# Optimization experiments

Hardware: AMD Instinct MI355X
Metric: run time of the kernel (lower is better)

## Reference

```python
import jax, jax.numpy as jnp
import numpy as np

H = 128
IN = 5
EPS = 1e-5


def lstm(x, Wih, Whh, bih, bhh):
    # x: [B,T,D]; PyTorch gate order i,f,g,o along 4H axis
    B, T, _ = x.shape
    xW = jnp.einsum('btd,gd->btg', x, Wih) + bih + bhh  # [B,T,4H]
    WhhT = Whh.T

    def step(carry, xt):
        h, c = carry
        g = xt + h @ WhhT
        i, f, gg, o = jnp.split(g, 4, axis=-1)
        i = jax.nn.sigmoid(i)
        f = jax.nn.sigmoid(f)
        gg = jnp.tanh(gg)
        o = jax.nn.sigmoid(o)
        c = f * c + i * gg
        h = o * jnp.tanh(c)
        return (h, c), h

    h0 = jnp.zeros((B, H), x.dtype)
    _, hs = jax.lax.scan(step, (h0, h0), jnp.swapaxes(xW, 0, 1))
    return jnp.swapaxes(hs, 0, 1)  # [B,T,H]


def batchnorm(x, gamma, beta):
    # training-mode BN over (batch, time) per channel; x: [B,T,H]
    mean = jnp.mean(x, axis=(0, 1))
    var = jnp.var(x, axis=(0, 1))
    return (x - mean) * (gamma * jax.lax.rsqrt(var + EPS)) + beta


def forward_one(x, Wih1, Whh1, bih1, bhh1, g1, b1, Wih2, Whh2, bih2, bhh2, g2, b2, fcW, fcb):
    out = lstm(x, Wih1, Whh1, bih1, bhh1)
    out = batchnorm(out, g1, b1)
    # dropout is identity (eval / deterministic reference)
    out = lstm(out, Wih2, Whh2, bih2, bhh2)
    out = batchnorm(out, g2, b2)
    emb = out[:, -1, :] @ fcW.T + fcb  # [B,128]
    norm = jnp.sqrt(jnp.sum(emb * emb, axis=1, keepdims=True))
    return emb / jnp.maximum(norm, 1e-12)  # F.normalize p=2


def setup_inputs() -> dict:
    key = jax.random.key(0)
    ks = jax.random.split(key, 20)
    B, T = 512, 128
    s_in = 1.0 / np.sqrt(H)
    d = {
        'a': jax.random.normal(ks[0], (B, T, IN), jnp.float32),
        'p': jax.random.normal(ks[1], (B, T, IN), jnp.float32),
        'n': jax.random.normal(ks[2], (B, T, IN), jnp.float32),
        'Wih1': jax.random.uniform(ks[3], (4 * H, IN), jnp.float32, -s_in, s_in),
        'Whh1': jax.random.uniform(ks[4], (4 * H, H), jnp.float32, -s_in, s_in),
        'bih1': jax.random.uniform(ks[5], (4 * H,), jnp.float32, -s_in, s_in),
        'bhh1': jax.random.uniform(ks[6], (4 * H,), jnp.float32, -s_in, s_in),
        'g1': jnp.ones((H,), jnp.float32),
        'b1': jnp.zeros((H,), jnp.float32),
        'Wih2': jax.random.uniform(ks[7], (4 * H, H), jnp.float32, -s_in, s_in),
        'Whh2': jax.random.uniform(ks[8], (4 * H, H), jnp.float32, -s_in, s_in),
        'bih2': jax.random.uniform(ks[9], (4 * H,), jnp.float32, -s_in, s_in),
        'bhh2': jax.random.uniform(ks[10], (4 * H,), jnp.float32, -s_in, s_in),
        'g2': jnp.ones((H,), jnp.float32),
        'b2': jnp.zeros((H,), jnp.float32),
        'fcW': jax.random.uniform(ks[11], (H, H), jnp.float32, -s_in, s_in),
        'fcb': jax.random.uniform(ks[12], (H,), jnp.float32, -s_in, s_in),
    }
    return d


def reference(a, p, n, Wih1, Whh1, bih1, bhh1, g1, b1, Wih2, Whh2, bih2, bhh2, g2, b2, fcW, fcb):
    f = lambda x: forward_one(x, Wih1, Whh1, bih1, bhh1, g1, b1, Wih2, Whh2, bih2, bhh2, g2, b2, fcW, fcb)
    return (f(a), f(p), f(n))
```

## Files before the change

kernel.cpp:

```cpp
#include <hip/hip_runtime.h>


typedef __attribute__((ext_vector_type(8))) _Float16 half8;
typedef __attribute__((ext_vector_type(4))) float f32x4;

#define TS 128
#define HID 128
#define NGATE 512
#define INV_N (1.0f/65536.0f)

#define BAR() asm volatile("s_waitcnt lgkmcnt(0)\n\ts_barrier" ::: "memory")

__device__ __forceinline__ float rcpf(float x) { return __builtin_amdgcn_rcpf(x); }
__device__ __forceinline__ float clamp20(float x) { return fminf(fmaxf(x, -20.0f), 20.0f); }

__device__ __forceinline__ _Float16 lstm_cell(float zi, float zf, float zg, float zo,
                                              float& c) {
  zg = clamp20(zg);
  float ei = __expf(-zi);
  float eg = __expf(-2.0f * zg);
  float ef = __expf(-zf);
  float fv = rcpf(1.0f + ef);
  float ig = (1.0f - eg) * rcpf((1.0f + ei) * (1.0f + eg));
  float cc = fv * c + ig;
  c = cc;
  float ccl = clamp20(cc);
  float eo = __expf(-zo);
  float ec = __expf(-2.0f * ccl);
  float hv = (1.0f - ec) * rcpf((1.0f + eo) * (1.0f + ec));
  return (_Float16)hv;
}


__global__ __launch_bounds__(512, 2) void lstm1_kernel(
    const float* __restrict__ xa, const float* __restrict__ xp,
    const float* __restrict__ xn,
    const float* __restrict__ Wih1, const float* __restrict__ Whh1,
    const float* __restrict__ bih1, const float* __restrict__ bhh1,
    _Float16* __restrict__ hs1,
    float* __restrict__ s1part, float* __restrict__ s1qpart) {
  const int wg = blockIdx.x;
  const int inp = wg >> 5;
  const int tid = threadIdx.x;
  const int w = tid >> 6;
  const int lane = tid & 63;
  const int l15 = lane & 15;
  const int quad = lane >> 4;
  const int col = w * 16 + l15;
  const int kb = quad * 8;

  __shared__ _Float16 hb[2][2048];
  __shared__ _Float16 xt[TS][128];

  const float* x = (inp == 0) ? xa : ((inp == 1) ? xp : xn);
  const int rloc = (wg & 31) * 16;

  for (int i = tid; i < 4096; i += 512) ((_Float16*)hb)[i] = (_Float16)0.0f;
  for (int i = tid; i < TS * 128; i += 512) ((_Float16*)xt)[i] = (_Float16)0.0f;
  __syncthreads();
  for (int i = tid; i < 10240; i += 512) {
    int r = i / 640, rem = i - r * 640;
    int t = rem / 5, d = rem - t * 5;
    xt[t][r * 8 + d] = (_Float16)x[(rloc + r) * 640 + rem];
  }

  half8 bh[4][4];
#pragma unroll
  for (int kt = 0; kt < 4; ++kt)
#pragma unroll
    for (int gt = 0; gt < 4; ++gt) {
      const float* src = &Whh1[(gt * 128 + col) * HID + kt * 32 + kb];
      half8 v;
#pragma unroll
      for (int j = 0; j < 8; ++j) v[j] = (_Float16)src[j];
      bh[kt][gt] = v;
    }
  half8 bx[4];
#pragma unroll
  for (int gt = 0; gt < 4; ++gt) {
    half8 v = {0, 0, 0, 0, 0, 0, 0, 0};
    if (quad == 0) {
#pragma unroll
      for (int j = 0; j < 5; ++j) v[j] = (_Float16)Wih1[(gt * 128 + col) * 5 + j];
    }
    bx[gt] = v;
  }
  f32x4 biasv[4];
#pragma unroll
  for (int gt = 0; gt < 4; ++gt) {
    float b = bih1[gt * 128 + col] + bhh1[gt * 128 + col];
    biasv[gt][0] = b; biasv[gt][1] = b; biasv[gt][2] = b; biasv[gt][3] = b;
  }

  const int rbase = (quad * 16 + l15) * 8;
  const int wbase = (w >> 1) * 512 + ((w & 1) * 2 + (l15 >> 3)) * 128 +
                    quad * 32 + (l15 & 7);
  _Float16* hs1w = hs1 + (size_t)wg * TS * 2048;

  float c[4] = {0, 0, 0, 0};
  float ssum = 0.0f, ssq = 0.0f;
  __syncthreads();

  half8 xv = {0, 0, 0, 0, 0, 0, 0, 0};
  if (quad == 0) xv = *(const half8*)&xt[0][l15 * 8];

  for (int t = 0; t < TS; ++t) {
    f32x4 acc[4];
#pragma unroll
    for (int gt = 0; gt < 4; ++gt)
      acc[gt] = __builtin_amdgcn_mfma_f32_16x16x32_f16(xv, bx[gt], biasv[gt], 0, 0, 0);
    if (t + 1 < TS && quad == 0)
      xv = *(const half8*)&xt[t + 1][l15 * 8];
    BAR();
    if (t > 0) {
      float2 cp = *(const float2*)&hb[t & 1][tid * 4];
      *(float2*)&hs1w[(size_t)(t - 1) * 2048 + tid * 4] = cp;
    }
#pragma unroll
    for (int kt = 0; kt < 4; ++kt) {
      half8 ah = *(const half8*)&hb[t & 1][kt * 512 + rbase];
#pragma unroll
      for (int gt = 0; gt < 4; ++gt)
        acc[gt] = __builtin_amdgcn_mfma_f32_16x16x32_f16(ah, bh[kt][gt], acc[gt], 0, 0, 0);
    }
    const int wb = (t + 1) & 1;
#pragma unroll
    for (int r = 0; r < 4; ++r) {
      _Float16 hh = lstm_cell(acc[0][r], acc[1][r], acc[2][r], acc[3][r], c[r]);
      float hr = (float)hh;
      ssum += hr; ssq += hr * hr;
      hb[wb][wbase + r * 8] = hh;
    }
  }
  BAR();
  {
    float2 cp = *(const float2*)&hb[0][tid * 4];
    *(float2*)&hs1w[(size_t)(TS - 1) * 2048 + tid * 4] = cp;
  }
  float s = ssum, q = ssq;
  s += __shfl_xor(s, 16); s += __shfl_xor(s, 32);
  q += __shfl_xor(q, 16); q += __shfl_xor(q, 32);
  if (quad == 0) {
    s1part[wg * HID + col] = s;
    s1qpart[wg * HID + col] = q;
  }
}

__global__ void mid_kernel(const float* __restrict__ s1part, const float* __restrict__ s1qpart,
                           const float* __restrict__ g1, const float* __restrict__ b1,
                           const float* __restrict__ Wih2,
                           const float* __restrict__ bih2, const float* __restrict__ bhh2,
                           _Float16* __restrict__ w2s, float* __restrict__ bias2eff) {
  int bid = blockIdx.x, tid = threadIdx.x;
  if (bid < 768) {
    int i0 = bid * 256;
    int inp = i0 >> 16, k = (i0 & 65535) >> 9;
    __shared__ float red[65];
    if (tid < 32) {
      red[tid] = s1part[(inp * 32 + tid) * HID + k];
      red[32 + tid] = s1qpart[(inp * 32 + tid) * HID + k];
    }
    __syncthreads();
    if (tid == 0) {
      float sm = 0.0f, sq = 0.0f;
      for (int j = 0; j < 32; ++j) { sm += red[j]; sq += red[32 + j]; }
      float m = sm * INV_N;
      float v = sq * INV_N - m * m;
      red[64] = g1[k] * rsqrtf(v + 1e-5f);
    }
    __syncthreads();
    float sc = red[64];
    int i = i0 + tid, g = i & 511;
    w2s[i] = (_Float16)(sc * Wih2[g * HID + k]);
  } else {
    int i = (bid - 768) * 256 + tid;
    int inp = i >> 9, g = i & 511;
    __shared__ float sc[128], sh[128];
    if (tid < 128) {
      float sm = 0.0f, sq = 0.0f;
      for (int j = 0; j < 32; ++j) {
        sm += s1part[(inp * 32 + j) * HID + tid];
        sq += s1qpart[(inp * 32 + j) * HID + tid];
      }
      float m = sm * INV_N;
      float v = sq * INV_N - m * m;
      float s = g1[tid] * rsqrtf(v + 1e-5f);
      sc[tid] = s;
      sh[tid] = b1[tid] - m * s;
    }
    __syncthreads();
    float acc = bih2[g] + bhh2[g];
    for (int h = 0; h < HID; ++h) acc += sh[h] * Wih2[g * HID + h];
    bias2eff[i] = acc;
  }
}

__global__ __launch_bounds__(512, 2) void lstm2_kernel(
    const _Float16* __restrict__ hs1,
    const _Float16* __restrict__ w2s,
    const float* __restrict__ Whh2,
    const float* __restrict__ bias2eff,
    _Float16* __restrict__ hlast,
    float* __restrict__ s2part, float* __restrict__ s2qpart) {
  const int wg = blockIdx.x;
  const int inp = wg >> 5;
  const int tid = threadIdx.x;
  const int w = tid >> 6;
  const int lane = tid & 63;
  const int l15 = lane & 15;
  const int quad = lane >> 4;
  const int col = w * 16 + l15;
  const int kb = quad * 8;

  __shared__ _Float16 hb[2][2048];
  for (int i = tid; i < 4096; i += 512) ((_Float16*)hb)[i] = (_Float16)0.0f;

  const _Float16* w2sI = w2s + (size_t)inp * HID * NGATE;
  half8 bh[4][4], bxw[4][4];
#pragma unroll
  for (int kt = 0; kt < 4; ++kt)
#pragma unroll
    for (int gt = 0; gt < 4; ++gt) {
      int gcol = gt * 128 + col;
      const float* ph = &Whh2[(size_t)gcol * HID + kt * 32 + kb];
      half8 vh, vx;
#pragma unroll
      for (int j = 0; j < 8; ++j) {
        vh[j] = (_Float16)ph[j];
        vx[j] = w2sI[(kt * 32 + kb + j) * NGATE + gcol];
      }
      bh[kt][gt] = vh;
      bxw[kt][gt] = vx;
    }
  f32x4 biasv[4];
#pragma unroll
  for (int gt = 0; gt < 4; ++gt) {
    float b = bias2eff[inp * NGATE + gt * 128 + col];
    biasv[gt][0] = b; biasv[gt][1] = b; biasv[gt][2] = b; biasv[gt][3] = b;
  }

  const int rbase = (quad * 16 + l15) * 8;
  const int wbase = (w >> 1) * 512 + ((w & 1) * 2 + (l15 >> 3)) * 128 +
                    quad * 32 + (l15 & 7);
  const _Float16* hg = hs1 + (size_t)wg * TS * 2048;

  half8 a2A[4], a2B[4];
#pragma unroll
  for (int kt = 0; kt < 4; ++kt) {
    a2A[kt] = *(const half8*)&hg[kt * 512 + rbase];
    a2B[kt] = *(const half8*)&hg[(size_t)2048 + kt * 512 + rbase];
  }

  float c[4] = {0, 0, 0, 0};
  float ssum = 0.0f, ssq = 0.0f;

  __syncthreads();

  auto step = [&](int t, half8 (&cur)[4]) {
    f32x4 acc[4];
#pragma unroll
    for (int gt = 0; gt < 4; ++gt)
      acc[gt] = __builtin_amdgcn_mfma_f32_16x16x32_f16(cur[0], bxw[0][gt], biasv[gt], 0, 0, 0);
#pragma unroll
    for (int kt = 1; kt < 4; ++kt)
#pragma unroll
      for (int gt = 0; gt < 4; ++gt)
        acc[gt] = __builtin_amdgcn_mfma_f32_16x16x32_f16(cur[kt], bxw[kt][gt], acc[gt], 0, 0, 0);
    if (t + 2 < TS) {
#pragma unroll
      for (int kt = 0; kt < 4; ++kt)
        cur[kt] = *(const half8*)&hg[(size_t)(t + 2) * 2048 + kt * 512 + rbase];
    }
    BAR();
#pragma unroll
    for (int kt = 0; kt < 4; ++kt) {
      half8 ah = *(const half8*)&hb[t & 1][kt * 512 + rbase];
#pragma unroll
      for (int gt = 0; gt < 4; ++gt)
        acc[gt] = __builtin_amdgcn_mfma_f32_16x16x32_f16(ah, bh[kt][gt], acc[gt], 0, 0, 0);
    }
    const int wb = (t + 1) & 1;
#pragma unroll
    for (int r = 0; r < 4; ++r) {
      _Float16 hh = lstm_cell(acc[0][r], acc[1][r], acc[2][r], acc[3][r], c[r]);
      float hr = (float)hh;
      ssum += hr; ssq += hr * hr;
      hb[wb][wbase + r * 8] = hh;
    }
  };

  for (int t = 0; t < TS; t += 2) {
    step(t, a2A);
    step(t + 1, a2B);
  }

  BAR();
  {
    float2 cp = *(const float2*)&hb[0][tid * 4];
    *(float2*)&hlast[(size_t)wg * 2048 + tid * 4] = cp;
  }
  float s = ssum, q = ssq;
  s += __shfl_xor(s, 16); s += __shfl_xor(s, 32);
  q += __shfl_xor(q, 16); q += __shfl_xor(q, 32);
  if (quad == 0) {
    s2part[wg * HID + col] = s;
    s2qpart[wg * HID + col] = q;
  }
}

__global__ __launch_bounds__(256, 1) void head_kernel(
    const _Float16* __restrict__ hlast,
    const float* __restrict__ s2part, const float* __restrict__ s2qpart,
    const float* __restrict__ g2, const float* __restrict__ b2,
    const float* __restrict__ fcW, const float* __restrict__ fcb,
    float* __restrict__ out) {
  const int wg = blockIdx.x;
  const int inp = wg >> 5;
  const int gr0 = wg * 16;
  const int tid = threadIdx.x;

  __shared__ float fcwT[128][132];
  __shared__ float bnh[16][132];
  __shared__ float s2[128], sh2[128];
  __shared__ float part[16][16];
  __shared__ float inv[16];

  if (tid < 128) {
    float sm = 0.0f, sq = 0.0f;
    for (int j = 0; j < 32; ++j) {
      sm += s2part[(inp * 32 + j) * HID + tid];
      sq += s2qpart[(inp * 32 + j) * HID + tid];
    }
    float m = sm * INV_N;
    float v = sq * INV_N - m * m;
    float s = g2[tid] * rsqrtf(v + 1e-5f);
    s2[tid] = s; sh2[tid] = b2[tid] - m * s;
  }
  for (int i = tid; i < 16384; i += 256) {
    int j = i >> 7, h = i & 127;
    fcwT[h][j] = fcW[i];
  }
  __syncthreads();
  {
    int row = tid >> 4, c0 = (tid & 15) * 8;
#pragma unroll
    for (int k = 0; k < 8; ++k) {
      int h = c0 + k;
      int ad = ((h >> 5) << 9) + (((h >> 3) & 3) << 7) + (row << 3) + (h & 7);
      bnh[row][h] = (float)hlast[(size_t)wg * 2048 + ad] * s2[h] + sh2[h];
    }
  }
  __syncthreads();
  const int row = tid >> 4, jl = tid & 15;
  float emb[8];
  float sq = 0.0f;
#pragma unroll
  for (int jj = 0; jj < 8; ++jj) {
    int j = jl + jj * 16;
    float acc = fcb[j];
    for (int h = 0; h < HID; ++h) acc += bnh[row][h] * fcwT[h][j];
    emb[jj] = acc; sq += acc * acc;
  }
  part[row][jl] = sq;
  __syncthreads();
  if (tid < 16) {
    float s = 0.0f;
    for (int k = 0; k < 16; ++k) s += part[tid][k];
    inv[tid] = 1.0f / fmaxf(sqrtf(s), 1e-12f);
  }
  __syncthreads();
#pragma unroll
  for (int jj = 0; jj < 8; ++jj)
    out[(size_t)(gr0 + row) * HID + jl + jj * 16] = emb[jj] * inv[row];
}

extern "C" void kernel_launch(void* const* d_in, const int* in_sizes, int n_in,
                              void* d_out, int out_size, void* d_ws, size_t ws_size,
                              hipStream_t stream) {
  const float* a    = (const float*)d_in[0];
  const float* p    = (const float*)d_in[1];
  const float* nn   = (const float*)d_in[2];
  const float* Wih1 = (const float*)d_in[3];
  const float* Whh1 = (const float*)d_in[4];
  const float* bih1 = (const float*)d_in[5];
  const float* bhh1 = (const float*)d_in[6];
  const float* g1   = (const float*)d_in[7];
  const float* b1   = (const float*)d_in[8];
  const float* Wih2 = (const float*)d_in[9];
  const float* Whh2 = (const float*)d_in[10];
  const float* bih2 = (const float*)d_in[11];
  const float* bhh2 = (const float*)d_in[12];
  const float* g2   = (const float*)d_in[13];
  const float* b2   = (const float*)d_in[14];
  const float* fcW  = (const float*)d_in[15];
  const float* fcb  = (const float*)d_in[16];

  char* ws = (char*)d_ws;
  float* s1part  = (float*)(ws + 0);
  float* s1qpart = (float*)(ws + 49152);
  float* s2part  = (float*)(ws + 98304);
  float* s2qpart = (float*)(ws + 147456);
  _Float16* w2s   = (_Float16*)(ws + 196608);
  float* bias2eff = (float*)(ws + 589824);
  _Float16* hlast = (_Float16*)(ws + 595968);
  _Float16* hs1   = (_Float16*)(ws + 989184);


  lstm1_kernel<<<96, 512, 0, stream>>>(a, p, nn, Wih1, Whh1, bih1, bhh1,
                                       hs1, s1part, s1qpart);
  mid_kernel<<<774, 256, 0, stream>>>(s1part, s1qpart, g1, b1, Wih2, bih2, bhh2,
                                      w2s, bias2eff);
  lstm2_kernel<<<96, 512, 0, stream>>>(hs1, w2s, Whh2, bias2eff,
                                       hlast, s2part, s2qpart);
  head_kernel<<<96, 256, 0, stream>>>(hlast, s2part, s2qpart, g2, b2, fcW, fcb,
                                      (float*)d_out);
}
```

Measured before the change: 375.1 us.

## Add prep kernel for padded x and transposed fp16 weights; split MFMA accumulation chains

A new prep kernel converts the inputs to a padded fp16 layout, transposes Whh1/Whh2 to fp16, and presums the layer-1 biases. lstm1 then streams x directly from global memory instead of staging it in LDS with a serial zero-fill and scatter. Both LSTM kernels split the recurrent MFMA chain into two independent accumulators that are summed at the end, shortening the dependent MFMA latency on each time step's critical path. The cost is an extra kernel launch with large global writes, plus per-step global loads of x in lstm1 in place of LDS reads.

```diff
diff --git a/kernel.cpp b/kernel.cpp
--- a/kernel.cpp
+++ b/kernel.cpp
@@ -32,15 +32,41 @@
 }
 
 
+__global__ void prep_all(const float* __restrict__ xa, const float* __restrict__ xp,
+                         const float* __restrict__ xn,
+                         const float* __restrict__ Whh1, const float* __restrict__ Whh2,
+                         const float* __restrict__ bih1, const float* __restrict__ bhh1,
+                         _Float16* __restrict__ xpad,
+                         _Float16* __restrict__ whhT1, _Float16* __restrict__ whhT2,
+                         float* __restrict__ b1c) {
+  int bid = blockIdx.x, tid = threadIdx.x;
+  if (bid < 6144) {
+    int i = bid * 256 + tid;
+    int tile = i >> 14, rem = i & 16383;
+    int t = rem >> 7, r = (rem >> 3) & 15, d = i & 7;
+    int inp = tile >> 5, rloc = (tile & 31) * 16;
+    const float* x = (inp == 0) ? xa : ((inp == 1) ? xp : xn);
+    xpad[i] = (d < 5) ? (_Float16)x[(rloc + r) * 640 + t * 5 + d] : (_Float16)0.0f;
+  } else if (bid < 6656) {
+    int i = (bid - 6144) * 256 + tid;
+    int which = i >> 16, idx = i & 65535;
+    int k = idx >> 9, g = idx & 511;
+    const float* src = which ? Whh2 : Whh1;
+    (which ? whhT2 : whhT1)[idx] = (_Float16)src[g * HID + k];
+  } else {
+    int i = (bid - 6656) * 256 + tid;
+    b1c[i] = bih1[i] + bhh1[i];
+  }
+}
+
 __global__ __launch_bounds__(512, 2) void lstm1_kernel(
-    const float* __restrict__ xa, const float* __restrict__ xp,
-    const float* __restrict__ xn,
-    const float* __restrict__ Wih1, const float* __restrict__ Whh1,
-    const float* __restrict__ bih1, const float* __restrict__ bhh1,
+    const _Float16* __restrict__ xpad,
+    const float* __restrict__ Wih1,
+    const float* __restrict__ b1c,
+    const _Float16* __restrict__ whhT,
     _Float16* __restrict__ hs1,
     float* __restrict__ s1part, float* __restrict__ s1qpart) {
   const int wg = blockIdx.x;
-  const int inp = wg >> 5;
   const int tid = threadIdx.x;
   const int w = tid >> 6;
   const int lane = tid & 63;
@@ -50,29 +76,17 @@
   const int kb = quad * 8;
 
   __shared__ _Float16 hb[2][2048];
-  __shared__ _Float16 xt[TS][128];
-
-  const float* x = (inp == 0) ? xa : ((inp == 1) ? xp : xn);
-  const int rloc = (wg & 31) * 16;
-
   for (int i = tid; i < 4096; i += 512) ((_Float16*)hb)[i] = (_Float16)0.0f;
-  for (int i = tid; i < TS * 128; i += 512) ((_Float16*)xt)[i] = (_Float16)0.0f;
-  __syncthreads();
-  for (int i = tid; i < 10240; i += 512) {
-    int r = i / 640, rem = i - r * 640;
-    int t = rem / 5, d = rem - t * 5;
-    xt[t][r * 8 + d] = (_Float16)x[(rloc + r) * 640 + rem];
-  }
 
   half8 bh[4][4];
 #pragma unroll
   for (int kt = 0; kt < 4; ++kt)
 #pragma unroll
     for (int gt = 0; gt < 4; ++gt) {
-      const float* src = &Whh1[(gt * 128 + col) * HID + kt * 32 + kb];
+      int gcol = gt * 128 + col;
       half8 v;
 #pragma unroll
-      for (int j = 0; j < 8; ++j) v[j] = (_Float16)src[j];
+      for (int j = 0; j < 8; ++j) v[j] = whhT[(kt * 32 + kb + j) * NGATE + gcol];
       bh[kt][gt] = v;
     }
   half8 bx[4];
@@ -88,9 +102,10 @@
   f32x4 biasv[4];
 #pragma unroll
   for (int gt = 0; gt < 4; ++gt) {
-    float b = bih1[gt * 128 + col] + bhh1[gt * 128 + col];
+    float b = b1c[gt * 128 + col];
     biasv[gt][0] = b; biasv[gt][1] = b; biasv[gt][2] = b; biasv[gt][3] = b;
   }
+  const f32x4 zero4 = {0, 0, 0, 0};
 
   const int rbase = (quad * 16 + l15) * 8;
   const int wbase = (w >> 1) * 512 + ((w & 1) * 2 + (l15 >> 3)) * 128 +
@@ -102,7 +117,7 @@
   __syncthreads();
 
   half8 xv = {0, 0, 0, 0, 0, 0, 0, 0};
-  if (quad == 0) xv = *(const half8*)&xt[0][l15 * 8];
+  if (quad == 0) xv = *(const half8*)&xpad[((size_t)(wg * TS) * 16 + l15) * 8];
 
   for (int t = 0; t < TS; ++t) {
     f32x4 acc[4];
@@ -110,19 +125,32 @@
     for (int gt = 0; gt < 4; ++gt)
       acc[gt] = __builtin_amdgcn_mfma_f32_16x16x32_f16(xv, bx[gt], biasv[gt], 0, 0, 0);
     if (t + 1 < TS && quad == 0)
-      xv = *(const half8*)&xt[t + 1][l15 * 8];
+      xv = *(const half8*)&xpad[((size_t)(wg * TS + t + 1) * 16 + l15) * 8];
     BAR();
+    half8 ah0 = *(const half8*)&hb[t & 1][0 * 512 + rbase];
+    half8 ah1 = *(const half8*)&hb[t & 1][1 * 512 + rbase];
+    half8 ah2 = *(const half8*)&hb[t & 1][2 * 512 + rbase];
+    half8 ah3 = *(const half8*)&hb[t & 1][3 * 512 + rbase];
+    f32x4 acc2[4];
+#pragma unroll
+    for (int gt = 0; gt < 4; ++gt)
+      acc[gt] = __builtin_amdgcn_mfma_f32_16x16x32_f16(ah0, bh[0][gt], acc[gt], 0, 0, 0);
+#pragma unroll
+    for (int gt = 0; gt < 4; ++gt)
+      acc2[gt] = __builtin_amdgcn_mfma_f32_16x16x32_f16(ah2, bh[2][gt], zero4, 0, 0, 0);
+#pragma unroll
+    for (int gt = 0; gt < 4; ++gt)
+      acc[gt] = __builtin_amdgcn_mfma_f32_16x16x32_f16(ah1, bh[1][gt], acc[gt], 0, 0, 0);
+#pragma unroll
+    for (int gt = 0; gt < 4; ++gt)
+      acc2[gt] = __builtin_amdgcn_mfma_f32_16x16x32_f16(ah3, bh[3][gt], acc2[gt], 0, 0, 0);
     if (t > 0) {
       float2 cp = *(const float2*)&hb[t & 1][tid * 4];
       *(float2*)&hs1w[(size_t)(t - 1) * 2048 + tid * 4] = cp;
     }
 #pragma unroll
-    for (int kt = 0; kt < 4; ++kt) {
-      half8 ah = *(const half8*)&hb[t & 1][kt * 512 + rbase];
-#pragma unroll
-      for (int gt = 0; gt < 4; ++gt)
-        acc[gt] = __builtin_amdgcn_mfma_f32_16x16x32_f16(ah, bh[kt][gt], acc[gt], 0, 0, 0);
-    }
+    for (int gt = 0; gt < 4; ++gt)
+      acc[gt] += acc2[gt];
     const int wb = (t + 1) & 1;
 #pragma unroll
     for (int r = 0; r < 4; ++r) {
@@ -175,7 +203,7 @@
   } else {
     int i = (bid - 768) * 256 + tid;
     int inp = i >> 9, g = i & 511;
-    __shared__ float sc[128], sh[128];
+    __shared__ float sh[128];
     if (tid < 128) {
       float sm = 0.0f, sq = 0.0f;
       for (int j = 0; j < 32; ++j) {
@@ -185,7 +213,6 @@
       float m = sm * INV_N;
       float v = sq * INV_N - m * m;
       float s = g1[tid] * rsqrtf(v + 1e-5f);
-      sc[tid] = s;
       sh[tid] = b1[tid] - m * s;
     }
     __syncthreads();
@@ -197,8 +224,8 @@
 
 __global__ __launch_bounds__(512, 2) void lstm2_kernel(
     const _Float16* __restrict__ hs1,
+    const _Float16* __restrict__ whhT2,
     const _Float16* __restrict__ w2s,
-    const float* __restrict__ Whh2,
     const float* __restrict__ bias2eff,
     _Float16* __restrict__ hlast,
     float* __restrict__ s2part, float* __restrict__ s2qpart) {
@@ -222,11 +249,10 @@
 #pragma unroll
     for (int gt = 0; gt < 4; ++gt) {
       int gcol = gt * 128 + col;
-      const float* ph = &Whh2[(size_t)gcol * HID + kt * 32 + kb];
       half8 vh, vx;
 #pragma unroll
       for (int j = 0; j < 8; ++j) {
-        vh[j] = (_Float16)ph[j];
+        vh[j] = whhT2[(kt * 32 + kb + j) * NGATE + gcol];
         vx[j] = w2sI[(kt * 32 + kb + j) * NGATE + gcol];
       }
       bh[kt][gt] = vh;
@@ -238,6 +264,7 @@
     float b = bias2eff[inp * NGATE + gt * 128 + col];
     biasv[gt][0] = b; biasv[gt][1] = b; biasv[gt][2] = b; biasv[gt][3] = b;
   }
+  const f32x4 zero4 = {0, 0, 0, 0};
 
   const int rbase = (quad * 16 + l15) * 8;
   const int wbase = (w >> 1) * 512 + ((w & 1) * 2 + (l15 >> 3)) * 128 +
@@ -257,28 +284,44 @@
   __syncthreads();
 
   auto step = [&](int t, half8 (&cur)[4]) {
-    f32x4 acc[4];
+    f32x4 acc[4], acc2[4];
 #pragma unroll
     for (int gt = 0; gt < 4; ++gt)
       acc[gt] = __builtin_amdgcn_mfma_f32_16x16x32_f16(cur[0], bxw[0][gt], biasv[gt], 0, 0, 0);
 #pragma unroll
-    for (int kt = 1; kt < 4; ++kt)
-#pragma unroll
-      for (int gt = 0; gt < 4; ++gt)
-        acc[gt] = __builtin_amdgcn_mfma_f32_16x16x32_f16(cur[kt], bxw[kt][gt], acc[gt], 0, 0, 0);
+    for (int gt = 0; gt < 4; ++gt)
+      acc2[gt] = __builtin_amdgcn_mfma_f32_16x16x32_f16(cur[2], bxw[2][gt], zero4, 0, 0, 0);
+#pragma unroll
+    for (int gt = 0; gt < 4; ++gt)
+      acc[gt] = __builtin_amdgcn_mfma_f32_16x16x32_f16(cur[1], bxw[1][gt], acc[gt], 0, 0, 0);
+#pragma unroll
+    for (int gt = 0; gt < 4; ++gt)
+      acc2[gt] = __builtin_amdgcn_mfma_f32_16x16x32_f16(cur[3], bxw[3][gt], acc2[gt], 0, 0, 0);
     if (t + 2 < TS) {
 #pragma unroll
       for (int kt = 0; kt < 4; ++kt)
         cur[kt] = *(const half8*)&hg[(size_t)(t + 2) * 2048 + kt * 512 + rbase];
     }
     BAR();
-#pragma unroll
-    for (int kt = 0; kt < 4; ++kt) {
-      half8 ah = *(const half8*)&hb[t & 1][kt * 512 + rbase];
-#pragma unroll
-      for (int gt = 0; gt < 4; ++gt)
-        acc[gt] = __builtin_amdgcn_mfma_f32_16x16x32_f16(ah, bh[kt][gt], acc[gt], 0, 0, 0);
-    }
+    half8 ah0 = *(const half8*)&hb[t & 1][0 * 512 + rbase];
+    half8 ah1 = *(const half8*)&hb[t & 1][1 * 512 + rbase];
+    half8 ah2 = *(const half8*)&hb[t & 1][2 * 512 + rbase];
+    half8 ah3 = *(const half8*)&hb[t & 1][3 * 512 + rbase];
+#pragma unroll
+    for (int gt = 0; gt < 4; ++gt)
+      acc[gt] = __builtin_amdgcn_mfma_f32_16x16x32_f16(ah0, bh[0][gt], acc[gt], 0, 0, 0);
+#pragma unroll
+    for (int gt = 0; gt < 4; ++gt)
+      acc2[gt] = __builtin_amdgcn_mfma_f32_16x16x32_f16(ah2, bh[2][gt], acc2[gt], 0, 0, 0);
+#pragma unroll
+    for (int gt = 0; gt < 4; ++gt)
+      acc[gt] = __builtin_amdgcn_mfma_f32_16x16x32_f16(ah1, bh[1][gt], acc[gt], 0, 0, 0);
+#pragma unroll
+    for (int gt = 0; gt < 4; ++gt)
+      acc2[gt] = __builtin_amdgcn_mfma_f32_16x16x32_f16(ah3, bh[3][gt], acc2[gt], 0, 0, 0);
+#pragma unroll
+    for (int gt = 0; gt < 4; ++gt)
+      acc[gt] += acc2[gt];
     const int wb = (t + 1) & 1;
 #pragma unroll
     for (int r = 0; r < 4; ++r) {
@@ -400,17 +443,23 @@
   float* s1qpart = (float*)(ws + 49152);
   float* s2part  = (float*)(ws + 98304);
   float* s2qpart = (float*)(ws + 147456);
-  _Float16* w2s   = (_Float16*)(ws + 196608);
-  float* bias2eff = (float*)(ws + 589824);
-  _Float16* hlast = (_Float16*)(ws + 595968);
-  _Float16* hs1   = (_Float16*)(ws + 989184);
-
-
-  lstm1_kernel<<<96, 512, 0, stream>>>(a, p, nn, Wih1, Whh1, bih1, bhh1,
+  float* b1c      = (float*)(ws + 196608);
+  float* bias2eff = (float*)(ws + 198656);
+  _Float16* whhT1 = (_Float16*)(ws + 204800);
+  _Float16* whhT2 = (_Float16*)(ws + 335872);
+  _Float16* w2s   = (_Float16*)(ws + 466944);
+  _Float16* hlast = (_Float16*)(ws + 860160);
+  _Float16* xpad  = (_Float16*)(ws + 1253376);
+  _Float16* hs1   = (_Float16*)(ws + 4399104);
+
+
+  prep_all<<<6658, 256, 0, stream>>>(a, p, nn, Whh1, Whh2, bih1, bhh1,
+                                     xpad, whhT1, whhT2, b1c);
+  lstm1_kernel<<<96, 512, 0, stream>>>(xpad, Wih1, b1c, whhT1,
                                        hs1, s1part, s1qpart);
   mid_kernel<<<774, 256, 0, stream>>>(s1part, s1qpart, g1, b1, Wih2, bih2, bhh2,
                                       w2s, bias2eff);
-  lstm2_kernel<<<96, 512, 0, stream>>>(hs1, w2s, Whh2, bias2eff,
+  lstm2_kernel<<<96, 512, 0, stream>>>(hs1, whhT2, w2s, bias2eff,
                                        hlast, s2part, s2qpart);
   head_kernel<<<96, 256, 0, stream>>>(hlast, s2part, s2qpart, g2, b2, fcW, fcb,
                                       (float*)d_out);
```

Measured after the change: 386.7 us. +3.1%, slower.
